# Optimization experiments

Hardware: AMD Instinct MI355X
Metric: run time of the kernel (lower is better)

Reference implementation:

```python
import jax, jax.numpy as jnp
import numpy as np

N_NODES = 50000
N_EDGES = 800000
NFEAT, NHID, NHEAD, NCLASS = 512, 64, 8, 40
NEG_SLOPE = 0.2  # LeakyReLU alpha from __init__


def setup_inputs() -> dict:
    key = jax.random.key(0)
    ks = jax.random.split(key, 8)
    glorot = lambda k, shape: jax.random.normal(k, shape, jnp.float32) * (2.0 / (shape[-2] + shape[-1])) ** 0.5
    return {
        "x": jax.random.normal(ks[0], (N_NODES, NFEAT), jnp.float32),
        "edge_list": jax.random.randint(ks[1], (2, N_EDGES), 0, N_NODES, jnp.int32),
        # nhead input-layer GATconv params: weight [H, nfeat, nhid], att [H, 2*nhid], bias [H, nhid]
        "W1": glorot(ks[2], (NHEAD, NFEAT, NHID)),
        "a1": jax.random.normal(ks[3], (NHEAD, 2 * NHID), jnp.float32) * 0.1,
        "b1": jnp.zeros((NHEAD, NHID), jnp.float32),
        # single output-head GATconv: [nhid*nhead, nclass]
        "W2": glorot(ks[4], (NHEAD * NHID, NCLASS)),
        "a2": jax.random.normal(ks[5], (2 * NCLASS,), jnp.float32) * 0.1,
        "b2": jnp.zeros((NCLASS,), jnp.float32),
    }


def _gat_layer(x, W, a, b, src, dst, n_nodes):
    """One GATconv head (eval mode, dropout = identity)."""
    h = x @ W                                  # [N, F]
    f = W.shape[-1]
    s_src = h @ a[:f]                          # [N] per-node src score
    s_dst = h @ a[f:]                          # [N] per-node dst score
    e = jax.nn.leaky_relu(s_src[src] + s_dst[dst], NEG_SLOPE)  # [E]
    # segment softmax over incoming edges of each dst node (numerically stable)
    m = jax.ops.segment_max(e, dst, num_segments=n_nodes)
    m = jax.lax.stop_gradient(jnp.where(jnp.isfinite(m), m, 0.0))
    w = jnp.exp(e - m[dst])
    denom = jax.ops.segment_sum(w, dst, num_segments=n_nodes)
    alpha = w / jnp.maximum(denom[dst], 1e-16)                 # [E]
    out = jax.ops.segment_sum(alpha[:, None] * h[src], dst, num_segments=n_nodes)
    return out + b


def reference(x, edge_list, W1, a1, b1, W2, a2, b2):
    n = x.shape[0]
    src, dst = edge_list[0], edge_list[1]
    # multi-head input layer, concat along feature dim
    heads = jax.vmap(lambda W, a, b: _gat_layer(x, W, a, b, src, dst, n))(W1, a1, b1)  # [H, N, nhid]
    h = jax.nn.elu(jnp.transpose(heads, (1, 0, 2)).reshape(n, -1))                      # [N, H*nhid]
    # single output head (mean over nhead_out=1)
    out = _gat_layer(h, W2, a2, b2, src, dst, n)                                        # [N, nclass]
    return jax.nn.log_softmax(out, axis=1)
```

## Files before the change

kernel.cpp:

```cpp
#include <hip/hip_runtime.h>
#include <math.h>

#define N_NODES 50000
#define N_EDGES 800000
#define NFEAT 512
#define NHID 64
#define NHEAD 8
#define NCLASS 40
#define NEG_SLOPE 0.2f

#define N_RT 3125
#define N_RT_PAD 3128
#define SCAN_NBLK 49

typedef __attribute__((ext_vector_type(8))) short short8;
typedef __attribute__((ext_vector_type(4))) short short4v;
typedef __attribute__((ext_vector_type(4))) float f32x4;

__device__ __forceinline__ float bf2f(short s) {
    return __uint_as_float(((unsigned)(unsigned short)s) << 16);
}
__device__ __forceinline__ short f2bf(float f) {
    unsigned u = __float_as_uint(f);
    unsigned r = (u + 0x7FFFu + ((u >> 16) & 1u)) >> 16;
    return (short)(unsigned short)r;
}
__device__ __forceinline__ int swz(int s) { return s ^ ((s >> 4) & 7); }



__global__ void count_deg(const int* __restrict__ el, int* __restrict__ deg) {
    int e = blockIdx.x * blockDim.x + threadIdx.x;
    if (e < N_EDGES) atomicAdd(&deg[el[N_EDGES + e]], 1);
}

__global__ __launch_bounds__(256) void scan1(const int* __restrict__ deg,
                                             int* __restrict__ loc,
                                             int* __restrict__ bsum) {
    int tid = threadIdx.x, lane = tid & 63, w = tid >> 6;
    int base = blockIdx.x * 1024 + tid * 4;
    int d0 = (base + 0 < N_NODES) ? deg[base + 0] : 0;
    int d1 = (base + 1 < N_NODES) ? deg[base + 1] : 0;
    int d2 = (base + 2 < N_NODES) ? deg[base + 2] : 0;
    int d3 = (base + 3 < N_NODES) ? deg[base + 3] : 0;
    int s0 = d0, s1 = s0 + d1, s2 = s1 + d2, s3 = s2 + d3;
    int t = s3;
#pragma unroll
    for (int d = 1; d < 64; d <<= 1) {
        int u = __shfl_up(t, d);
        if (lane >= d) t += u;
    }
    __shared__ int wsum[4];
    if (lane == 63) wsum[w] = t;
    __syncthreads();
    int woff = 0;
#pragma unroll
    for (int j = 0; j < 4; ++j) woff += (j < w) ? wsum[j] : 0;
    int excl = woff + t - s3;
    if (base + 0 < N_NODES) loc[base + 0] = excl + s0;
    if (base + 1 < N_NODES) loc[base + 1] = excl + s1;
    if (base + 2 < N_NODES) loc[base + 2] = excl + s2;
    if (base + 3 < N_NODES) loc[base + 3] = excl + s3;
    if (tid == 255) bsum[blockIdx.x] = woff + t;
}

__global__ __launch_bounds__(256) void scan3(const int* __restrict__ deg,
                                             const int* __restrict__ loc,
                                             const int* __restrict__ bsum,
                                             int* __restrict__ ptr,
                                             int* __restrict__ cursor) {
    __shared__ int sOff;
    if (threadIdx.x < 64) {
        int lane = threadIdx.x;
        int v = (lane < SCAN_NBLK && lane < (int)blockIdx.x) ? bsum[lane] : 0;
#pragma unroll
        for (int m = 1; m < 64; m <<= 1) v += __shfl_xor(v, m);
        if (lane == 0) sOff = v;
    }
    __syncthreads();
    int off = sOff;
    int base = blockIdx.x * 1024 + threadIdx.x * 4;
    if (blockIdx.x == 0 && threadIdx.x == 0) ptr[0] = 0;
#pragma unroll
    for (int k = 0; k < 4; ++k) {
        int i = base + k;
        if (i < N_NODES) {
            int P = off + loc[i];
            ptr[i + 1] = P;
            cursor[i] = P - deg[i];
        }
    }
}

__global__ void scatter_k(const int* __restrict__ el, int* __restrict__ cursor,
                          int* __restrict__ esrc) {
    int e = blockIdx.x * blockDim.x + threadIdx.x;
    if (e >= N_EDGES) return;
    int dst = el[N_EDGES + e];
    int p = atomicAdd(&cursor[dst], 1);
    esrc[p] = el[e];
}

__global__ __launch_bounds__(256) void pack_w(const float* __restrict__ W1,
                                              const float* __restrict__ W2,
                                              short* __restrict__ Wp1,
                                              short* __restrict__ Wp2) {
    int t = blockIdx.x * 256 + threadIdx.x;
    if (t < 32768) {
        int l = t & 63, ct = (t >> 6) & 7, ks = (t >> 9) & 15, g = t >> 13;
        int c = g * 128 + ct * 16 + (l & 15);
        int head = c >> 6, f = c & 63;
        int k0 = ks * 32 + (l >> 4) * 8;
        short8 o;
#pragma unroll
        for (int j = 0; j < 8; ++j)
            o[j] = f2bf(W1[(size_t)head * NFEAT * NHID + (k0 + j) * NHID + f]);
        *(short8*)(Wp1 + (size_t)t * 8) = o;
    } else if (t < 32768 + 3072) {
        int u = t - 32768;
        int l = u & 63;
        int kc = u >> 6;
        int ct2 = kc % 3, ks = kc / 3;
        int col = ct2 * 16 + (l & 15);
        short8 o;
#pragma unroll
        for (int j = 0; j < 8; ++j) {
            int kp = ks * 32 + (l >> 4) * 8 + j;
            int head = kp >> 6, fp = kp & 63;
            int l15 = fp >> 2, ctp = fp & 3;
            int ct = ((head & 1) << 2) | ctp;
            int gg = head >> 1;
            int orig_k = gg * 128 + ct * 16 + l15;
            o[j] = (col < NCLASS) ? f2bf(W2[(size_t)orig_k * NCLASS + col]) : (short)0;
        }
        *(short8*)(Wp2 + (size_t)u * 8) = o;
    }
}

__global__ __launch_bounds__(256, 2) void gemm1(const float* __restrict__ x,
                                                const short* __restrict__ Wp1,
                                                const float* __restrict__ a1,
                                                short* __restrict__ h1p,
                                                float* __restrict__ s1s,
                                                float* __restrict__ s1d) {
    __shared__ short As[2 * 16 * 64 * 8];
    int w = threadIdx.x >> 6, l = threadIdx.x & 63;
    int g = w;
    int rt0 = blockIdx.x * 2;
    int row0 = rt0 * 16;

#pragma unroll
    for (int u = 0; u < 8; ++u) {
        int idx = threadIdx.x + u * 256;
        int rl = idx >> 6, cg = idx & 63;
        int row = row0 + rl;
        short8 o;
        if (row < N_NODES) {
            const float* p = x + (size_t)row * NFEAT + cg * 8;
            f32x4 v0 = __builtin_nontemporal_load((const f32x4*)p);
            f32x4 v1 = __builtin_nontemporal_load((const f32x4*)(p + 4));
            o[0] = f2bf(v0[0]); o[1] = f2bf(v0[1]); o[2] = f2bf(v0[2]); o[3] = f2bf(v0[3]);
            o[4] = f2bf(v1[0]); o[5] = f2bf(v1[1]); o[6] = f2bf(v1[2]); o[7] = f2bf(v1[3]);
        } else {
#pragma unroll
            for (int j = 0; j < 8; ++j) o[j] = 0;
        }
        int rtl = rl >> 4, rloc = rl & 15, ks = cg >> 2, sub = cg & 3;
        int lane = rloc + sub * 16;
        int slot = (rtl * 16 + ks) * 64 + lane;
        *(short8*)(As + swz(slot) * 8) = o;
    }
    __syncthreads();

    f32x4 acc[2][8];
#pragma unroll
    for (int i = 0; i < 2; ++i)
#pragma unroll
        for (int ct = 0; ct < 8; ++ct) acc[i][ct] = (f32x4){0.f, 0.f, 0.f, 0.f};

    const short* bP = Wp1 + (size_t)g * 16 * 4096 + l * 8;
    short8 b0[8], b1[8], n0[8], n1[8];
#pragma unroll
    for (int ct = 0; ct < 8; ++ct) b0[ct] = *(const short8*)(bP + ct * 512);
#pragma unroll
    for (int ct = 0; ct < 8; ++ct) b1[ct] = *(const short8*)(bP + 4096 + ct * 512);

    for (int kk = 0; kk < 8; ++kk) {
        int ks0 = 2 * kk, ks1 = 2 * kk + 1;
        int kp0 = (ks0 + 2 < 16) ? ks0 + 2 : 15;
        int kp1 = (ks1 + 2 < 16) ? ks1 + 2 : 15;
#pragma unroll
        for (int ct = 0; ct < 8; ++ct) n0[ct] = *(const short8*)(bP + kp0 * 4096 + ct * 512);
#pragma unroll
        for (int ct = 0; ct < 8; ++ct) n1[ct] = *(const short8*)(bP + kp1 * 4096 + ct * 512);

        short8 a00 = *(const short8*)(As + swz(ks0 * 64 + l) * 8);
        short8 a01 = *(const short8*)(As + swz((16 + ks0) * 64 + l) * 8);
#pragma unroll
        for (int ct = 0; ct < 8; ++ct) {
            acc[0][ct] = __builtin_amdgcn_mfma_f32_16x16x32_bf16(a00, b0[ct], acc[0][ct], 0, 0, 0);
            acc[1][ct] = __builtin_amdgcn_mfma_f32_16x16x32_bf16(a01, b0[ct], acc[1][ct], 0, 0, 0);
        }
        short8 a10 = *(const short8*)(As + swz(ks1 * 64 + l) * 8);
        short8 a11 = *(const short8*)(As + swz((16 + ks1) * 64 + l) * 8);
#pragma unroll
        for (int ct = 0; ct < 8; ++ct) {
            acc[0][ct] = __builtin_amdgcn_mfma_f32_16x16x32_bf16(a10, b1[ct], acc[0][ct], 0, 0, 0);
            acc[1][ct] = __builtin_amdgcn_mfma_f32_16x16x32_bf16(a11, b1[ct], acc[1][ct], 0, 0, 0);
        }
#pragma unroll
        for (int ct = 0; ct < 8; ++ct) { b0[ct] = n0[ct]; b1[ct] = n1[ct]; }
    }

    float avs[8], avd[8];
#pragma unroll
    for (int ct = 0; ct < 8; ++ct) {
        int head = 2 * g + (ct >> 2);
        int f = (ct & 3) * 16 + (l & 15);
        avs[ct] = a1[head * 128 + f];
        avd[ct] = a1[head * 128 + 64 + f];
    }
    int l15 = l & 15;
    int rbase = (l >> 4) * 4;
#pragma unroll
    for (int i = 0; i < 2; ++i)
#pragma unroll
        for (int r = 0; r < 4; ++r) {
            int row = (rt0 + i) * 16 + rbase + r;
            float ps0 = 0.f, pd0 = 0.f, ps1 = 0.f, pd1 = 0.f;
#pragma unroll
            for (int ct = 0; ct < 4; ++ct) {
                ps0 += acc[i][ct][r] * avs[ct];
                pd0 += acc[i][ct][r] * avd[ct];
            }
#pragma unroll
            for (int ct = 4; ct < 8; ++ct) {
                ps1 += acc[i][ct][r] * avs[ct];
                pd1 += acc[i][ct][r] * avd[ct];
            }
#pragma unroll
            for (int mask = 1; mask < 16; mask <<= 1) {
                ps0 += __shfl_xor(ps0, mask);
                pd0 += __shfl_xor(pd0, mask);
                ps1 += __shfl_xor(ps1, mask);
                pd1 += __shfl_xor(pd1, mask);
            }
            if (row < N_NODES) {
                if (l15 == 0) {
                    s1s[row * 8 + 2 * g]     = ps0;
                    s1d[row * 8 + 2 * g]     = pd0;
                    s1s[row * 8 + 2 * g + 1] = ps1;
                    s1d[row * 8 + 2 * g + 1] = pd1;
                }
                short4v o0, o1;
#pragma unroll
                for (int c = 0; c < 4; ++c) { o0[c] = f2bf(acc[i][c][r]); o1[c] = f2bf(acc[i][4 + c][r]); }
                size_t base = (size_t)row * 512 + g * 128 + l15 * 4;
                *(short4v*)(h1p + base) = o0;
                *(short4v*)(h1p + base + 64) = o1;
            }
        }
}

__global__ __launch_bounds__(256, 4) void att1(const int* __restrict__ ptr,
                                               const int* __restrict__ esrc,
                                               const float* __restrict__ s1s,
                                               const float* __restrict__ s1d,
                                               const short* __restrict__ h1p,
                                               const float* __restrict__ b1,
                                               short* __restrict__ hcat) {
    int n = blockIdx.x * 4 + (threadIdx.x >> 6);
    int l = threadIdx.x & 63;
    if (n >= N_NODES) return;
    int beg = ptr[n], end = ptr[n + 1];
    int h = l >> 3;
    float sd = s1d[n * 8 + h];
    float den = 0.f;
    float acc[8] = {0.f, 0.f, 0.f, 0.f, 0.f, 0.f, 0.f, 0.f};
    const short* hb = h1p + l * 8;
    if (beg < end) {
        int last = end - 1;
        int p1 = (beg + 1 <= last) ? beg + 1 : last;
        int p2 = (beg + 2 <= last) ? beg + 2 : last;
        int p3 = (beg + 3 <= last) ? beg + 3 : last;
        int s0 = esrc[beg], s1 = esrc[p1], s2 = esrc[p2], s3 = esrc[p3];
        short8 v0 = *(const short8*)(hb + (size_t)s0 * 512);
        short8 v1 = *(const short8*)(hb + (size_t)s1 * 512);
        short8 v2 = *(const short8*)(hb + (size_t)s2 * 512);
        short8 v3 = *(const short8*)(hb + (size_t)s3 * 512);
        float ss0 = s1s[s0 * 8 + h], ss1 = s1s[s1 * 8 + h];
        float ss2 = s1s[s2 * 8 + h], ss3 = s1s[s3 * 8 + h];
        for (int i = beg; i < end; i += 4) {
            int ni = i + 4;
            int t0 = s0, t1 = s1, t2 = s2, t3 = s3;
            short8 u0 = v0, u1 = v1, u2 = v2, u3 = v3;
            float ts0 = ss0, ts1 = ss1, ts2 = ss2, ts3 = ss3;
            if (ni < end) {
                int q1 = (ni + 1 <= last) ? ni + 1 : last;
                int q2 = (ni + 2 <= last) ? ni + 2 : last;
                int q3 = (ni + 3 <= last) ? ni + 3 : last;
                t0 = esrc[ni]; t1 = esrc[q1]; t2 = esrc[q2]; t3 = esrc[q3];
                u0 = *(const short8*)(hb + (size_t)t0 * 512);
                u1 = *(const short8*)(hb + (size_t)t1 * 512);
                u2 = *(const short8*)(hb + (size_t)t2 * 512);
                u3 = *(const short8*)(hb + (size_t)t3 * 512);
                ts0 = s1s[t0 * 8 + h]; ts1 = s1s[t1 * 8 + h];
                ts2 = s1s[t2 * 8 + h]; ts3 = s1s[t3 * 8 + h];
            }
            float e0 = ss0 + sd, e1 = ss1 + sd, e2 = ss2 + sd, e3 = ss3 + sd;
            e0 = fmaxf(e0, NEG_SLOPE * e0);
            e1 = fmaxf(e1, NEG_SLOPE * e1);
            e2 = fmaxf(e2, NEG_SLOPE * e2);
            e3 = fmaxf(e3, NEG_SLOPE * e3);
            float w0 = __expf(e0);
            float w1 = (i + 1 < end) ? __expf(e1) : 0.f;
            float w2 = (i + 2 < end) ? __expf(e2) : 0.f;
            float w3 = (i + 3 < end) ? __expf(e3) : 0.f;
            den += (w0 + w1) + (w2 + w3);
#pragma unroll
            for (int j = 0; j < 8; ++j)
                acc[j] += (w0 * bf2f(v0[j]) + w1 * bf2f(v1[j])) +
                          (w2 * bf2f(v2[j]) + w3 * bf2f(v3[j]));
            s0 = t0; s1 = t1; s2 = t2; s3 = t3;
            v0 = u0; v1 = u1; v2 = u2; v3 = u3;
            ss0 = ts0; ss1 = ts1; ss2 = ts2; ss3 = ts3;
        }
    }
    float rden = 1.f / fmaxf(den, 1e-16f);
    short8 o;
#pragma unroll
    for (int j = 0; j < 8; ++j) {
        int forig = (j & 3) * 16 + (l & 7) * 2 + (j >> 2);
        float v = acc[j] * rden + b1[h * 64 + forig];
        v = v > 0.f ? v : (__expf(v) - 1.f);
        o[j] = f2bf(v);
    }
    *(short8*)(hcat + (size_t)n * 512 + l * 8) = o;
}

__global__ __launch_bounds__(256) void gemm2(const short* __restrict__ hcat,
                                             const short* __restrict__ Wp2,
                                             const float* __restrict__ a2,
                                             short* __restrict__ h2,
                                             float* __restrict__ s2s,
                                             float* __restrict__ s2d) {
    int w = threadIdx.x >> 6, l = threadIdx.x & 63;
    int rt = blockIdx.x * 4 + w;
    int arow = rt * 16 + (l & 15);
    const short* aBase = hcat + (size_t)arow * 512 + (l >> 4) * 8;
    f32x4 acc[3];
#pragma unroll
    for (int ct = 0; ct < 3; ++ct) acc[ct] = (f32x4){0.f, 0.f, 0.f, 0.f};
#pragma unroll 2
    for (int ks = 0; ks < 16; ++ks) {
        short8 a = *(const short8*)(aBase + ks * 32);
        const short* bp = Wp2 + (size_t)(ks * 3) * 512 + l * 8;
#pragma unroll
        for (int ct = 0; ct < 3; ++ct) {
            short8 b = *(const short8*)(bp + ct * 512);
            acc[ct] = __builtin_amdgcn_mfma_f32_16x16x32_bf16(a, b, acc[ct], 0, 0, 0);
        }
    }
    float ps[4] = {0.f, 0.f, 0.f, 0.f}, pd[4] = {0.f, 0.f, 0.f, 0.f};
    int cl = l & 15, rb = (l >> 4) * 4;
#pragma unroll
    for (int ct = 0; ct < 3; ++ct) {
        int col = ct * 16 + cl;
        if (col < NCLASS) {
#pragma unroll
            for (int r = 0; r < 4; ++r) {
                ps[r] += acc[ct][r] * a2[col];
                pd[r] += acc[ct][r] * a2[NCLASS + col];
                int row = rt * 16 + rb + r;
                if (row < N_NODES) h2[(size_t)row * NCLASS + col] = f2bf(acc[ct][r]);
            }
        }
    }
#pragma unroll
    for (int mask = 1; mask < 16; mask <<= 1)
#pragma unroll
        for (int r = 0; r < 4; ++r) {
            ps[r] += __shfl_xor(ps[r], mask);
            pd[r] += __shfl_xor(pd[r], mask);
        }
    if (cl == 0) {
#pragma unroll
        for (int r = 0; r < 4; ++r) {
            int row = rt * 16 + rb + r;
            if (row < N_NODES) { s2s[row] = ps[r]; s2d[row] = pd[r]; }
        }
    }
}

__global__ __launch_bounds__(256, 4) void att2(const int* __restrict__ ptr,
                                               const int* __restrict__ esrc,
                                               const float* __restrict__ s2s,
                                               const float* __restrict__ s2d,
                                               const short* __restrict__ h2,
                                               const float* __restrict__ b2,
                                               float* __restrict__ out) {
    int n = blockIdx.x * 4 + (threadIdx.x >> 6);
    int l = threadIdx.x & 63;
    if (n >= N_NODES) return;
    int beg = ptr[n], end = ptr[n + 1];
    float sd = s2d[n];
    float den = 0.f, acc = 0.f;
    int last = end - 1;
    bool act = (l < NCLASS);
    for (int i = beg; i < end; i += 4) {
        int i1 = (i + 1 <= last) ? i + 1 : last;
        int i2 = (i + 2 <= last) ? i + 2 : last;
        int i3 = (i + 3 <= last) ? i + 3 : last;
        int s0 = esrc[i], s1 = esrc[i1], s2 = esrc[i2], s3 = esrc[i3];
        float h0 = act ? bf2f(h2[(size_t)s0 * NCLASS + l]) : 0.f;
        float h1 = act ? bf2f(h2[(size_t)s1 * NCLASS + l]) : 0.f;
        float hh2 = act ? bf2f(h2[(size_t)s2 * NCLASS + l]) : 0.f;
        float h3 = act ? bf2f(h2[(size_t)s3 * NCLASS + l]) : 0.f;
        float e0 = s2s[s0] + sd;
        float e1 = s2s[s1] + sd;
        float e2 = s2s[s2] + sd;
        float e3 = s2s[s3] + sd;
        e0 = fmaxf(e0, NEG_SLOPE * e0);
        e1 = fmaxf(e1, NEG_SLOPE * e1);
        e2 = fmaxf(e2, NEG_SLOPE * e2);
        e3 = fmaxf(e3, NEG_SLOPE * e3);
        float w0 = __expf(e0);
        float w1 = (i + 1 < end) ? __expf(e1) : 0.f;
        float w2 = (i + 2 < end) ? __expf(e2) : 0.f;
        float w3 = (i + 3 < end) ? __expf(e3) : 0.f;
        den += (w0 + w1) + (w2 + w3);
        acc += (w0 * h0 + w1 * h1) + (w2 * hh2 + w3 * h3);
    }
    float v = act ? acc / fmaxf(den, 1e-16f) + b2[l] : -INFINITY;
    float mx = v;
#pragma unroll
    for (int o = 32; o; o >>= 1) mx = fmaxf(mx, __shfl_down(mx, o));
    mx = __shfl(mx, 0);
    float ex = act ? __expf(v - mx) : 0.f;
    float s = ex;
#pragma unroll
    for (int o = 32; o; o >>= 1) s += __shfl_down(s, o);
    s = __shfl(s, 0);
    float ls = __logf(s);
    if (act) out[(size_t)n * NCLASS + l] = v - mx - ls;
}


extern "C" void kernel_launch(void* const* d_in, const int* in_sizes, int n_in,
                              void* d_out, int out_size, void* d_ws, size_t ws_size,
                              hipStream_t stream) {
    const float* x  = (const float*)d_in[0];
    const int*   el = (const int*)d_in[1];
    const float* W1 = (const float*)d_in[2];
    const float* a1 = (const float*)d_in[3];
    const float* b1 = (const float*)d_in[4];
    const float* W2 = (const float*)d_in[5];
    const float* a2 = (const float*)d_in[6];
    const float* b2 = (const float*)d_in[7];
    float* out = (float*)d_out;

    short* sbase = (short*)d_ws;
    short* hcat  = sbase + 25624576;
    short* h1p   = sbase + 51249152;
    short* Wp1   = sbase + 76849152;
    short* Wp2   = sbase + 77111296;
    short* h2    = sbase + 77135872;
    float* fbase = (float*)(sbase + 79135872);
    float* s1s   = fbase;
    float* s1d   = fbase + 400000;
    float* s2s   = fbase + 800000;
    float* s2d   = fbase + 850000;
    int*   ibase = (int*)(fbase + 900000);
    int*   deg    = ibase;
    int*   ptr    = ibase + 50000;
    int*   cursor = ibase + 100001;
    int*   esrc   = ibase + 150001;
    int*   loc    = ibase + 950001;
    int*   bsum   = ibase + 1000001;

    hipMemsetAsync(deg, 0, (size_t)N_NODES * 4, stream);
    count_deg<<<(N_EDGES + 255) / 256, 256, 0, stream>>>(el, deg);
    scan1<<<SCAN_NBLK, 256, 0, stream>>>(deg, loc, bsum);
    scan3<<<SCAN_NBLK, 256, 0, stream>>>(deg, loc, bsum, ptr, cursor);
    scatter_k<<<(N_EDGES + 255) / 256, 256, 0, stream>>>(el, cursor, esrc);

    pack_w<<<140, 256, 0, stream>>>(W1, W2, Wp1, Wp2);

    gemm1<<<N_RT_PAD / 2, 256, 0, stream>>>(x, Wp1, a1, h1p, s1s, s1d);
    att1<<<(N_NODES + 3) / 4, 256, 0, stream>>>(ptr, esrc, s1s, s1d, h1p, b1, hcat);

    gemm2<<<N_RT_PAD / 4, 256, 0, stream>>>(hcat, Wp2, a2, h2, s2s, s2d);
    att2<<<(N_NODES + 3) / 4, 256, 0, stream>>>(ptr, esrc, s2s, s2d, h2, b2, out);
}
```

Baseline: 522.6 us.

## Split first-layer attention aggregation into two head-half passes

The first-layer attention kernel now runs twice, and each launch handles four of the eight heads. Each wavefront gathers 8-byte slices of the neighbour feature rows instead of 16-byte slices, so each pass touches half of h1p. The aim is a smaller gather working set per pass and more lanes per node-head. The explicit software prefetch of the next four edges is also dropped for a simpler loop. In exchange, edge indices and pointers are read twice, there is an extra launch, and less memory-level parallelism comes from prefetching.

```diff
diff --git a/kernel.cpp b/kernel.cpp
--- a/kernel.cpp
+++ b/kernel.cpp
@@ -268,74 +268,54 @@
                                                const float* __restrict__ s1d,
                                                const short* __restrict__ h1p,
                                                const float* __restrict__ b1,
-                                               short* __restrict__ hcat) {
+                                               short* __restrict__ hcat,
+                                               int h0) {
     int n = blockIdx.x * 4 + (threadIdx.x >> 6);
     int l = threadIdx.x & 63;
     if (n >= N_NODES) return;
     int beg = ptr[n], end = ptr[n + 1];
-    int h = l >> 3;
+    int h = h0 + (l >> 4);
     float sd = s1d[n * 8 + h];
     float den = 0.f;
-    float acc[8] = {0.f, 0.f, 0.f, 0.f, 0.f, 0.f, 0.f, 0.f};
-    const short* hb = h1p + l * 8;
-    if (beg < end) {
-        int last = end - 1;
-        int p1 = (beg + 1 <= last) ? beg + 1 : last;
-        int p2 = (beg + 2 <= last) ? beg + 2 : last;
-        int p3 = (beg + 3 <= last) ? beg + 3 : last;
-        int s0 = esrc[beg], s1 = esrc[p1], s2 = esrc[p2], s3 = esrc[p3];
-        short8 v0 = *(const short8*)(hb + (size_t)s0 * 512);
-        short8 v1 = *(const short8*)(hb + (size_t)s1 * 512);
-        short8 v2 = *(const short8*)(hb + (size_t)s2 * 512);
-        short8 v3 = *(const short8*)(hb + (size_t)s3 * 512);
-        float ss0 = s1s[s0 * 8 + h], ss1 = s1s[s1 * 8 + h];
-        float ss2 = s1s[s2 * 8 + h], ss3 = s1s[s3 * 8 + h];
-        for (int i = beg; i < end; i += 4) {
-            int ni = i + 4;
-            int t0 = s0, t1 = s1, t2 = s2, t3 = s3;
-            short8 u0 = v0, u1 = v1, u2 = v2, u3 = v3;
-            float ts0 = ss0, ts1 = ss1, ts2 = ss2, ts3 = ss3;
-            if (ni < end) {
-                int q1 = (ni + 1 <= last) ? ni + 1 : last;
-                int q2 = (ni + 2 <= last) ? ni + 2 : last;
-                int q3 = (ni + 3 <= last) ? ni + 3 : last;
-                t0 = esrc[ni]; t1 = esrc[q1]; t2 = esrc[q2]; t3 = esrc[q3];
-                u0 = *(const short8*)(hb + (size_t)t0 * 512);
-                u1 = *(const short8*)(hb + (size_t)t1 * 512);
-                u2 = *(const short8*)(hb + (size_t)t2 * 512);
-                u3 = *(const short8*)(hb + (size_t)t3 * 512);
-                ts0 = s1s[t0 * 8 + h]; ts1 = s1s[t1 * 8 + h];
-                ts2 = s1s[t2 * 8 + h]; ts3 = s1s[t3 * 8 + h];
-            }
-            float e0 = ss0 + sd, e1 = ss1 + sd, e2 = ss2 + sd, e3 = ss3 + sd;
-            e0 = fmaxf(e0, NEG_SLOPE * e0);
-            e1 = fmaxf(e1, NEG_SLOPE * e1);
-            e2 = fmaxf(e2, NEG_SLOPE * e2);
-            e3 = fmaxf(e3, NEG_SLOPE * e3);
-            float w0 = __expf(e0);
-            float w1 = (i + 1 < end) ? __expf(e1) : 0.f;
-            float w2 = (i + 2 < end) ? __expf(e2) : 0.f;
-            float w3 = (i + 3 < end) ? __expf(e3) : 0.f;
-            den += (w0 + w1) + (w2 + w3);
-#pragma unroll
-            for (int j = 0; j < 8; ++j)
-                acc[j] += (w0 * bf2f(v0[j]) + w1 * bf2f(v1[j])) +
-                          (w2 * bf2f(v2[j]) + w3 * bf2f(v3[j]));
-            s0 = t0; s1 = t1; s2 = t2; s3 = t3;
-            v0 = u0; v1 = u1; v2 = u2; v3 = u3;
-            ss0 = ts0; ss1 = ts1; ss2 = ts2; ss3 = ts3;
-        }
+    float acc[4] = {0.f, 0.f, 0.f, 0.f};
+    const short* hb = h1p + h0 * 64 + l * 4;
+    int last = end - 1;
+    for (int i = beg; i < end; i += 4) {
+        int i1 = (i + 1 <= last) ? i + 1 : last;
+        int i2 = (i + 2 <= last) ? i + 2 : last;
+        int i3 = (i + 3 <= last) ? i + 3 : last;
+        int s0 = esrc[i], s1 = esrc[i1], s2 = esrc[i2], s3 = esrc[i3];
+        short4v v0 = *(const short4v*)(hb + (size_t)s0 * 512);
+        short4v v1 = *(const short4v*)(hb + (size_t)s1 * 512);
+        short4v v2 = *(const short4v*)(hb + (size_t)s2 * 512);
+        short4v v3 = *(const short4v*)(hb + (size_t)s3 * 512);
+        float e0 = s1s[s0 * 8 + h] + sd;
+        float e1 = s1s[s1 * 8 + h] + sd;
+        float e2 = s1s[s2 * 8 + h] + sd;
+        float e3 = s1s[s3 * 8 + h] + sd;
+        e0 = fmaxf(e0, NEG_SLOPE * e0);
+        e1 = fmaxf(e1, NEG_SLOPE * e1);
+        e2 = fmaxf(e2, NEG_SLOPE * e2);
+        e3 = fmaxf(e3, NEG_SLOPE * e3);
+        float w0 = __expf(e0);
+        float w1 = (i + 1 < end) ? __expf(e1) : 0.f;
+        float w2 = (i + 2 < end) ? __expf(e2) : 0.f;
+        float w3 = (i + 3 < end) ? __expf(e3) : 0.f;
+        den += (w0 + w1) + (w2 + w3);
+#pragma unroll
+        for (int j = 0; j < 4; ++j)
+            acc[j] += (w0 * bf2f(v0[j]) + w1 * bf2f(v1[j])) +
+                      (w2 * bf2f(v2[j]) + w3 * bf2f(v3[j]));
     }
     float rden = 1.f / fmaxf(den, 1e-16f);
-    short8 o;
-#pragma unroll
-    for (int j = 0; j < 8; ++j) {
-        int forig = (j & 3) * 16 + (l & 7) * 2 + (j >> 2);
-        float v = acc[j] * rden + b1[h * 64 + forig];
+    short4v o;
+#pragma unroll
+    for (int j = 0; j < 4; ++j) {
+        float v = acc[j] * rden + b1[h * 64 + (j << 4) + (l & 15)];
         v = v > 0.f ? v : (__expf(v) - 1.f);
         o[j] = f2bf(v);
     }
-    *(short8*)(hcat + (size_t)n * 512 + l * 8) = o;
+    *(short4v*)(hcat + (size_t)n * 512 + h0 * 64 + l * 4) = o;
 }
 
 __global__ __launch_bounds__(256) void gemm2(const short* __restrict__ hcat,
@@ -487,7 +467,8 @@
     pack_w<<<140, 256, 0, stream>>>(W1, W2, Wp1, Wp2);
 
     gemm1<<<N_RT_PAD / 2, 256, 0, stream>>>(x, Wp1, a1, h1p, s1s, s1d);
-    att1<<<(N_NODES + 3) / 4, 256, 0, stream>>>(ptr, esrc, s1s, s1d, h1p, b1, hcat);
+    att1<<<(N_NODES + 3) / 4, 256, 0, stream>>>(ptr, esrc, s1s, s1d, h1p, b1, hcat, 0);
+    att1<<<(N_NODES + 3) / 4, 256, 0, stream>>>(ptr, esrc, s1s, s1d, h1p, b1, hcat, 4);
 
     gemm2<<<N_RT_PAD / 4, 256, 0, stream>>>(hcat, Wp2, a2, h2, s2s, s2d);
     att2<<<(N_NODES + 3) / 4, 256, 0, stream>>>(ptr, esrc, s2s, s2d, h2, b2, out);
```

Measured after the change: 531.4 us. No clear change (+1.7%).
